# Performance work log

Measured on AMD Instinct MI355X. Metric: run time of the kernel, lower is better.

## Reference

```python
import jax, jax.numpy as jnp
import numpy as np

H_RENDER = 640   # hard-coded render resolution in the torch forward
W_RENDER = 640
OUT_H = 128      # self.height
OUT_W = 128      # self.width
NUM_VERTS = 778  # MANO hand mesh
NUM_FACES = 1538
BATCH = 4
BG_DEPTH = 1e10  # z-buffer background, clamped to 100 afterwards


def setup_inputs() -> dict:
    key = jax.random.key(0)
    k1, k2, k3 = jax.random.split(key, 3)
    # screen-space x,y in [0, 640), positive depth z
    xy = jax.random.uniform(k1, (BATCH, NUM_VERTS, 2), minval=0.0, maxval=640.0)
    z = jax.random.uniform(k2, (BATCH, NUM_VERTS, 1), minval=0.3, maxval=1.5)
    vertices = jnp.concatenate([xy, z], axis=-1).astype(jnp.float32)
    faces = jax.random.randint(k3, (NUM_FACES, 3), 0, NUM_VERTS)
    # right_hand=True: swap face columns 0 and 1 (winding flip), as in __init__
    faces = faces[:, jnp.array([1, 0, 2])].astype(jnp.int64)
    return {"vertices": vertices, "faces": faces}


def _edge(ax, ay, bx, by, px, py):
    # signed area of (a, b, p); standard rasterizer edge function
    return (bx - ax) * (py - ay) - (by - ay) * (px - ax)


def _rasterize(face_vertices):
    # face_vertices: [B, F, 3(vertex), 3(x,y,z)] -> z-buffer depth map [B, H, W]
    B = face_vertices.shape[0]
    ys, xs = jnp.meshgrid(
        jnp.arange(H_RENDER, dtype=jnp.float32) + 0.5,
        jnp.arange(W_RENDER, dtype=jnp.float32) + 0.5,
        indexing='ij',
    )  # pixel centers, [H, W]

    def step(zbuf, tri):
        # tri: [B, 3, 3] -> per-vertex coords broadcast to [B, 1, 1]
        x = tri[:, :, 0][:, :, None, None]
        y = tri[:, :, 1][:, :, None, None]
        z = tri[:, :, 2][:, :, None, None]
        x0, x1, x2 = x[:, 0], x[:, 1], x[:, 2]
        y0, y1, y2 = y[:, 0], y[:, 1], y[:, 2]
        z0, z1, z2 = z[:, 0], z[:, 1], z[:, 2]
        e0 = _edge(x1, y1, x2, y2, xs, ys)  # weight of v0
        e1 = _edge(x2, y2, x0, y0, xs, ys)  # weight of v1
        e2 = _edge(x0, y0, x1, y1, xs, ys)  # weight of v2
        area = _edge(x0, y0, x1, y1, x2, y2)  # [B,1,1]
        s = jnp.sign(area)
        valid = jnp.abs(area) > 1e-12
        inside = (e0 * s >= 0) & (e1 * s >= 0) & (e2 * s >= 0) & valid
        safe_area = jnp.where(valid, area, 1.0)
        zpix = (e0 * z0 + e1 * z1 + e2 * z2) / safe_area  # barycentric depth
        cand = jnp.where(inside, zpix, jnp.float32(BG_DEPTH))
        return jnp.minimum(zbuf, cand), None

    zbuf0 = jnp.full((B, H_RENDER, W_RENDER), BG_DEPTH, dtype=jnp.float32)
    zbuf, _ = jax.lax.scan(step, zbuf0, jnp.swapaxes(face_vertices, 0, 1))
    return zbuf


def reference(vertices, faces):
    B = vertices.shape[0]
    F = faces.shape[0]
    # vertex gather: vertices[:, faces.view(-1), 0:3].view(B, F, 3, 3)
    fv = vertices[:, faces.reshape(-1), 0:3].reshape(B, F, 3, 3)
    dm = _rasterize(fv)
    dm = jnp.minimum(dm, 100.0)  # torch.clamp(max=100.0)
    # bilinear resize, align_corners=False (half-pixel), no antialias, like F.interpolate
    resized = jax.image.resize(dm[:, None], (B, 1, OUT_H, OUT_W), method='linear', antialias=False)
    return resized[:, 0]
```

## Files before the change

### kernel.cpp

```cpp
#include <hip/hip_runtime.h>


#pragma clang fp contract(off)

#define H_OUT 128
#define W_OUT 128
#define NV 778
#define NF 1538
#define NB 4
#define NCHUNK 25
#define NFP (NCHUNK * 64)
#define BG100 0x42C80000u


__global__ __launch_bounds__(256) void prep_kernel(
    const float* __restrict__ verts,
    const int* __restrict__ faces,
    float* __restrict__ bbox,
    float* __restrict__ data,
    unsigned int* __restrict__ outu)
{
    int t = blockIdx.x * 256 + threadIdx.x;
    outu[t] = BG100;
    if (t >= NB * NFP) return;
    int b = t / NFP;
    int f = t - b * NFP;
    float* bb = bbox + (size_t)t * 4;
    if (f >= NF) {
        bb[0] = 1e30f; bb[1] = -1e30f; bb[2] = 1e30f; bb[3] = -1e30f;
        return;
    }
    int i0 = faces[f * 3 + 0];
    int i1 = faces[f * 3 + 1];
    int i2 = faces[f * 3 + 2];
    const float* vb = verts + (size_t)b * NV * 3;
    float x0 = vb[i0 * 3 + 0], y0 = vb[i0 * 3 + 1], z0 = vb[i0 * 3 + 2];
    float x1 = vb[i1 * 3 + 0], y1 = vb[i1 * 3 + 1], z1 = vb[i1 * 3 + 2];
    float x2 = vb[i2 * 3 + 0], y2 = vb[i2 * 3 + 1], z2 = vb[i2 * 3 + 2];

    float dx12 = x2 - x1, dy12 = y2 - y1;
    float dx02 = x0 - x2, dy02 = y0 - y2;
    float dx01 = x1 - x0, dy01 = y1 - y0;
    float y20 = y2 - y0, x20 = x2 - x0;
    float area = dx01 * y20 - dy01 * x20;

    float s = 0.0f;
    if (fabsf(area) > 1e-12f) s = (area > 0.0f) ? 1.0f : -1.0f;

    float xmin = fminf(fminf(x0, x1), x2), xmax = fmaxf(fmaxf(x0, x1), x2);
    float ymin = fminf(fminf(y0, y1), y2), ymax = fmaxf(fmaxf(y0, y1), y2);
    if (s == 0.0f) { xmin = 1e30f; xmax = -1e30f; }

    bb[0] = xmin; bb[1] = xmax; bb[2] = ymin; bb[3] = ymax;

    float* o = data + (size_t)t * 16;
    o[0] = s * dx12; o[1] = s * dy12;
    o[2] = s * dx02; o[3] = s * dy02;
    o[4] = s * dx01; o[5] = s * dy01;
    o[6] = x0;  o[7] = y0;  o[8] = x1;  o[9] = y1;  o[10] = x2; o[11] = y2;
    o[12] = z0; o[13] = z1; o[14] = z2; o[15] = s * area;
}

__global__ __launch_bounds__(64) void raster_kernel(
    const float* __restrict__ bbox,
    const float* __restrict__ data,
    unsigned int* __restrict__ outu)
{
    int blk = blockIdx.x;
    int tile  = blk & 63;
    int b     = (blk >> 6) & 3;
    int chunk = blk >> 8;
    int lane = threadIdx.x;

    int tx = tile & 7, ty = tile >> 3;
    int col = lane & 15;
    int rg  = lane >> 4;
    int j = tx * 16 + col;
    int i0r = ty * 16 + rg;
    float px  = 5.0f * (float)j + 2.5f;
    float py0 = 5.0f * (float)i0r + 2.5f;

    float px_lo = 80.0f * (float)tx + 2.5f, px_hi = px_lo + 75.0f;
    float py_lo = 80.0f * (float)ty + 2.5f, py_hi = py_lo + 75.0f;

    int gbase = b * NFP + chunk * 64;
    float4 bb = *(const float4*)&bbox[(size_t)(gbase + lane) * 4];
    bool ov = !(bb.x > px_hi || bb.y < px_lo || bb.z > py_hi || bb.w < py_lo);
    unsigned long long mask = __ballot(ov);

    float nb0 = 1e10f, ab0 = 1.0f;
    float nb1 = 1e10f, ab1 = 1.0f;
    float nb2 = 1e10f, ab2 = 1.0f;
    float nb3 = 1e10f, ab3 = 1.0f;

    while (mask) {
        int f0 = __builtin_ctzll(mask); mask &= mask - 1;
        int f1 = mask ? __builtin_ctzll(mask) : f0;
        mask &= mask - 1;

        int u0 = __builtin_amdgcn_readfirstlane(f0);
        int u1 = __builtin_amdgcn_readfirstlane(f1);
        const float4* p0 = (const float4*)(data + (size_t)(gbase + u0) * 16);
        const float4* p1 = (const float4*)(data + (size_t)(gbase + u1) * 16);
        float4 A0 = p0[0], B0 = p0[1], C0 = p0[2], D0 = p0[3];
        float4 A1 = p1[0], B1 = p1[1], C1 = p1[2], D1 = p1[3];

        #pragma unroll
        for (int k = 0; k < 4; ++k) {
            float py = py0 + 20.0f * (float)k;
            float* nbp = (k == 0) ? &nb0 : (k == 1) ? &nb1 : (k == 2) ? &nb2 : &nb3;
            float* abp = (k == 0) ? &ab0 : (k == 1) ? &ab1 : (k == 2) ? &ab2 : &ab3;
            float nb = *nbp, ab = *abp;

            float e0 = A0.x * (py - C0.y) - A0.y * (px - C0.x);
            float e1 = A0.z * (py - C0.w) - A0.w * (px - C0.z);
            float e2 = B0.x * (py - B0.w) - B0.y * (px - B0.z);
            bool in0 = (e0 >= 0.0f) & (e1 >= 0.0f) & (e2 >= 0.0f);
            float n0 = ((e0 * D0.x) + (e1 * D0.y)) + (e2 * D0.z);
            bool t0 = in0 & (n0 * ab < nb * D0.w);
            nb = t0 ? n0 : nb;  ab = t0 ? D0.w : ab;

            float h0 = A1.x * (py - C1.y) - A1.y * (px - C1.x);
            float h1 = A1.z * (py - C1.w) - A1.w * (px - C1.z);
            float h2 = B1.x * (py - B1.w) - B1.y * (px - B1.z);
            bool in1 = (h0 >= 0.0f) & (h1 >= 0.0f) & (h2 >= 0.0f);
            float n1 = ((h0 * D1.x) + (h1 * D1.y)) + (h2 * D1.z);
            bool t1 = in1 & (n1 * ab < nb * D1.w);
            nb = t1 ? n1 : nb;  ab = t1 ? D1.w : ab;

            *nbp = nb; *abp = ab;
        }
    }

    unsigned int* slot0 = &outu[(size_t)b * (H_OUT * W_OUT) + i0r * W_OUT + j];
    #pragma unroll
    for (int k = 0; k < 4; ++k) {
        float nb = (k == 0) ? nb0 : (k == 1) ? nb1 : (k == 2) ? nb2 : nb3;
        float ab = (k == 0) ? ab0 : (k == 1) ? ab1 : (k == 2) ? ab2 : ab3;
        float z = nb / ab;
        z += 0.0f;
        if (z < 1e9f)
            atomicMin(slot0 + k * 4 * W_OUT, __float_as_uint(fminf(z, 100.0f)));
    }
}

extern "C" void kernel_launch(void* const* d_in, const int* in_sizes, int n_in,
                              void* d_out, int out_size, void* d_ws, size_t ws_size,
                              hipStream_t stream) {
    const float* verts = (const float*)d_in[0];
    const int*   faces = (const int*)d_in[1];
    float* out = (float*)d_out;
    float* bbox = (float*)d_ws;
    float* data = bbox + (size_t)NB * NFP * 4;

    prep_kernel<<<256, 256, 0, stream>>>(verts, faces, bbox, data,
                                         (unsigned int*)out);
    raster_kernel<<<NCHUNK * NB * 64, 64, 0, stream>>>(
        bbox, data, (unsigned int*)out);
}
```

Baseline: 97.02 us.

## Add per-tile binning pass and rasterize compacted face lists in fixed pieces

Adds a bin kernel that, for each batch and tile, compacts the indices of faces whose bounding boxes overlap the tile into a list padded to a multiple of 32 with a dummy face. The raster kernel then launches 64 pieces per bin, each processing exactly 32 listed faces with a fully unrolled loop and early exit for empty pieces. Previously every chunk block did a bbox test and a variable-length ballot loop over 64 faces. This is meant to remove wasted blocks and divergent loop control. In exchange it adds a third kernel launch, extra workspace traffic, and a fixed capacity for face lists.

Measured after the change: 147.7 us. 52.2% more time.

```diff
diff --git a/kernel.cpp b/kernel.cpp
--- a/kernel.cpp
+++ b/kernel.cpp
@@ -8,8 +8,9 @@
 #define NV 778
 #define NF 1538
 #define NB 4
-#define NCHUNK 25
-#define NFP (NCHUNK * 64)
+#define NFP 1600
+#define CAP 2048
+#define NPIECE 64
 #define BG100 0x42C80000u
 
 
@@ -26,8 +27,14 @@
     int b = t / NFP;
     int f = t - b * NFP;
     float* bb = bbox + (size_t)t * 4;
+    float* o  = data + (size_t)t * 16;
     if (f >= NF) {
         bb[0] = 1e30f; bb[1] = -1e30f; bb[2] = 1e30f; bb[3] = -1e30f;
+        o[0] = 0.0f; o[1] = 1.0f;
+        o[2] = 0.0f; o[3] = 0.0f; o[4] = 0.0f; o[5] = 0.0f;
+        o[6] = 0.0f; o[7] = 0.0f; o[8] = -1e30f; o[9] = 0.0f;
+        o[10] = 0.0f; o[11] = 0.0f; o[12] = 0.0f; o[13] = 0.0f; o[14] = 0.0f;
+        o[15] = 1.0f;
         return;
     }
     int i0 = faces[f * 3 + 0];
@@ -53,7 +60,6 @@
 
     bb[0] = xmin; bb[1] = xmax; bb[2] = ymin; bb[3] = ymax;
 
-    float* o = data + (size_t)t * 16;
     o[0] = s * dx12; o[1] = s * dy12;
     o[2] = s * dx02; o[3] = s * dy02;
     o[4] = s * dx01; o[5] = s * dy01;
@@ -61,83 +67,114 @@
     o[12] = z0; o[13] = z1; o[14] = z2; o[15] = s * area;
 }
 
+__global__ __launch_bounds__(64) void bin_kernel(
+    const float* __restrict__ bbox,
+    unsigned int* __restrict__ list,
+    unsigned int* __restrict__ count)
+{
+    int bin = blockIdx.x;
+    int b = bin >> 6, tile = bin & 63;
+    int tx = tile & 7, ty = tile >> 3;
+    int lane = threadIdx.x;
+
+    float px_lo = 80.0f * (float)tx + 2.5f, px_hi = px_lo + 75.0f;
+    float py_lo = 80.0f * (float)ty + 2.5f, py_hi = py_lo + 75.0f;
+
+    unsigned int* lp = list + (size_t)bin * CAP;
+    unsigned int base = 0;
+    for (int c = 0; c < NFP / 64; ++c) {
+        int f = c * 64 + lane;
+        float4 bb = *(const float4*)&bbox[(size_t)(b * NFP + f) * 4];
+        bool ov = !(bb.x > px_hi || bb.y < px_lo ||
+                    bb.z > py_hi || bb.w < py_lo);
+        unsigned long long m = __ballot(ov);
+        if (ov) {
+            int pre = __popcll(m & ((1ull << lane) - 1ull));
+            lp[base + pre] = (unsigned int)f;
+        }
+        base += (unsigned int)__popcll(m);
+    }
+    unsigned int padN = (32u - (base & 31u)) & 31u;
+    if ((unsigned int)lane < padN) lp[base + lane] = NFP - 1;
+    if (lane == 0) count[bin] = base + padN;
+}
+
+__device__ __forceinline__ void face_pair(
+    const float* __restrict__ data, int gb, unsigned int fa, unsigned int fb,
+    float px, float py0, float nb[4], float ab[4])
+{
+    int u0 = __builtin_amdgcn_readfirstlane((int)fa);
+    int u1 = __builtin_amdgcn_readfirstlane((int)fb);
+    const float4* p0 = (const float4*)(data + (size_t)(gb + u0) * 16);
+    const float4* p1 = (const float4*)(data + (size_t)(gb + u1) * 16);
+    float4 A0 = p0[0], B0 = p0[1], C0 = p0[2], D0 = p0[3];
+    float4 A1 = p1[0], B1 = p1[1], C1 = p1[2], D1 = p1[3];
+
+    #pragma unroll
+    for (int k = 0; k < 4; ++k) {
+        float py = py0 + 20.0f * (float)k;
+        float nbk = nb[k], abk = ab[k];
+
+        float e0 = A0.x * (py - C0.y) - A0.y * (px - C0.x);
+        float e1 = A0.z * (py - C0.w) - A0.w * (px - C0.z);
+        float e2 = B0.x * (py - B0.w) - B0.y * (px - B0.z);
+        bool in0 = (e0 >= 0.0f) & (e1 >= 0.0f) & (e2 >= 0.0f);
+        float n0 = ((e0 * D0.x) + (e1 * D0.y)) + (e2 * D0.z);
+        bool t0 = in0 & (n0 * abk < nbk * D0.w);
+        nbk = t0 ? n0 : nbk;  abk = t0 ? D0.w : abk;
+
+        float h0 = A1.x * (py - C1.y) - A1.y * (px - C1.x);
+        float h1 = A1.z * (py - C1.w) - A1.w * (px - C1.z);
+        float h2 = B1.x * (py - B1.w) - B1.y * (px - B1.z);
+        bool in1 = (h0 >= 0.0f) & (h1 >= 0.0f) & (h2 >= 0.0f);
+        float n1 = ((h0 * D1.x) + (h1 * D1.y)) + (h2 * D1.z);
+        bool t1 = in1 & (n1 * abk < nbk * D1.w);
+        nbk = t1 ? n1 : nbk;  abk = t1 ? D1.w : abk;
+
+        nb[k] = nbk; ab[k] = abk;
+    }
+}
+
 __global__ __launch_bounds__(64) void raster_kernel(
-    const float* __restrict__ bbox,
     const float* __restrict__ data,
+    const unsigned int* __restrict__ list,
+    const unsigned int* __restrict__ count,
     unsigned int* __restrict__ outu)
 {
     int blk = blockIdx.x;
-    int tile  = blk & 63;
-    int b     = (blk >> 6) & 3;
-    int chunk = blk >> 8;
+    int bin = blk >> 6, piece = blk & 63;
+    unsigned int cnt = count[bin];
+    if ((unsigned int)(piece * 32) >= cnt) return;
+
+    int b = bin >> 6, tile = bin & 63;
+    int tx = tile & 7, ty = tile >> 3;
     int lane = threadIdx.x;
-
-    int tx = tile & 7, ty = tile >> 3;
     int col = lane & 15;
     int rg  = lane >> 4;
     int j = tx * 16 + col;
     int i0r = ty * 16 + rg;
     float px  = 5.0f * (float)j + 2.5f;
     float py0 = 5.0f * (float)i0r + 2.5f;
-
-    float px_lo = 80.0f * (float)tx + 2.5f, px_hi = px_lo + 75.0f;
-    float py_lo = 80.0f * (float)ty + 2.5f, py_hi = py_lo + 75.0f;
-
-    int gbase = b * NFP + chunk * 64;
-    float4 bb = *(const float4*)&bbox[(size_t)(gbase + lane) * 4];
-    bool ov = !(bb.x > px_hi || bb.y < px_lo || bb.z > py_hi || bb.w < py_lo);
-    unsigned long long mask = __ballot(ov);
-
-    float nb0 = 1e10f, ab0 = 1.0f;
-    float nb1 = 1e10f, ab1 = 1.0f;
-    float nb2 = 1e10f, ab2 = 1.0f;
-    float nb3 = 1e10f, ab3 = 1.0f;
-
-    while (mask) {
-        int f0 = __builtin_ctzll(mask); mask &= mask - 1;
-        int f1 = mask ? __builtin_ctzll(mask) : f0;
-        mask &= mask - 1;
-
-        int u0 = __builtin_amdgcn_readfirstlane(f0);
-        int u1 = __builtin_amdgcn_readfirstlane(f1);
-        const float4* p0 = (const float4*)(data + (size_t)(gbase + u0) * 16);
-        const float4* p1 = (const float4*)(data + (size_t)(gbase + u1) * 16);
-        float4 A0 = p0[0], B0 = p0[1], C0 = p0[2], D0 = p0[3];
-        float4 A1 = p1[0], B1 = p1[1], C1 = p1[2], D1 = p1[3];
-
-        #pragma unroll
-        for (int k = 0; k < 4; ++k) {
-            float py = py0 + 20.0f * (float)k;
-            float* nbp = (k == 0) ? &nb0 : (k == 1) ? &nb1 : (k == 2) ? &nb2 : &nb3;
-            float* abp = (k == 0) ? &ab0 : (k == 1) ? &ab1 : (k == 2) ? &ab2 : &ab3;
-            float nb = *nbp, ab = *abp;
-
-            float e0 = A0.x * (py - C0.y) - A0.y * (px - C0.x);
-            float e1 = A0.z * (py - C0.w) - A0.w * (px - C0.z);
-            float e2 = B0.x * (py - B0.w) - B0.y * (px - B0.z);
-            bool in0 = (e0 >= 0.0f) & (e1 >= 0.0f) & (e2 >= 0.0f);
-            float n0 = ((e0 * D0.x) + (e1 * D0.y)) + (e2 * D0.z);
-            bool t0 = in0 & (n0 * ab < nb * D0.w);
-            nb = t0 ? n0 : nb;  ab = t0 ? D0.w : ab;
-
-            float h0 = A1.x * (py - C1.y) - A1.y * (px - C1.x);
-            float h1 = A1.z * (py - C1.w) - A1.w * (px - C1.z);
-            float h2 = B1.x * (py - B1.w) - B1.y * (px - B1.z);
-            bool in1 = (h0 >= 0.0f) & (h1 >= 0.0f) & (h2 >= 0.0f);
-            float n1 = ((h0 * D1.x) + (h1 * D1.y)) + (h2 * D1.z);
-            bool t1 = in1 & (n1 * ab < nb * D1.w);
-            nb = t1 ? n1 : nb;  ab = t1 ? D1.w : ab;
-
-            *nbp = nb; *abp = ab;
-        }
+    int gb = b * NFP;
+
+    const uint4* lp = (const uint4*)(list + (size_t)bin * CAP + piece * 32);
+    uint4 I[8];
+    #pragma unroll
+    for (int q = 0; q < 8; ++q) I[q] = lp[q];
+
+    float nb[4] = {1e10f, 1e10f, 1e10f, 1e10f};
+    float ab[4] = {1.0f, 1.0f, 1.0f, 1.0f};
+
+    #pragma unroll
+    for (int q = 0; q < 8; ++q) {
+        face_pair(data, gb, I[q].x, I[q].y, px, py0, nb, ab);
+        face_pair(data, gb, I[q].z, I[q].w, px, py0, nb, ab);
     }
 
     unsigned int* slot0 = &outu[(size_t)b * (H_OUT * W_OUT) + i0r * W_OUT + j];
     #pragma unroll
     for (int k = 0; k < 4; ++k) {
-        float nb = (k == 0) ? nb0 : (k == 1) ? nb1 : (k == 2) ? nb2 : nb3;
-        float ab = (k == 0) ? ab0 : (k == 1) ? ab1 : (k == 2) ? ab2 : ab3;
-        float z = nb / ab;
+        float z = nb[k] / ab[k];
         z += 0.0f;
         if (z < 1e9f)
             atomicMin(slot0 + k * 4 * W_OUT, __float_as_uint(fminf(z, 100.0f)));
@@ -152,9 +189,12 @@
     float* out = (float*)d_out;
     float* bbox = (float*)d_ws;
     float* data = bbox + (size_t)NB * NFP * 4;
+    unsigned int* list = (unsigned int*)(data + (size_t)NB * NFP * 16);
+    unsigned int* count = list + (size_t)256 * CAP;
 
     prep_kernel<<<256, 256, 0, stream>>>(verts, faces, bbox, data,
                                          (unsigned int*)out);
-    raster_kernel<<<NCHUNK * NB * 64, 64, 0, stream>>>(
-        bbox, data, (unsigned int*)out);
-}
+    bin_kernel<<<256, 64, 0, stream>>>(bbox, list, count);
+    raster_kernel<<<256 * NPIECE, 64, 0, stream>>>(
+        data, list, count, (unsigned int*)out);
+}
```
